# Kernel optimization log

Measured on AMD Instinct MI355X. Metric: run time of the kernel, lower is better.

The kernel has to match this reference:

```python
import jax, jax.numpy as jnp
import numpy as np

B, C, H, W = 32, 512, 64, 64
P = 8            # partition (window) size
HEAD_DIM = 32
N_HEADS = C // HEAD_DIM  # 16
MLP_RATIO = 4
LN_EPS = 1e-5


def _rel_pos_index(p):
    # Swin/MaxViT-style relative position index for a p x p window -> [p*p, p*p]
    coords = np.stack(np.meshgrid(np.arange(p), np.arange(p), indexing='ij'), 0).reshape(2, -1)
    rel = coords[:, :, None] - coords[:, None, :]          # [2, pp, pp]
    rel = rel.transpose(1, 2, 0) + (p - 1)                 # shift to >= 0
    idx = rel[..., 0] * (2 * p - 1) + rel[..., 1]          # [pp, pp]
    return jnp.asarray(idx, jnp.int32)


def setup_inputs() -> dict:
    key = jax.random.key(0)
    ks = jax.random.split(key, 10)
    s = 0.02
    d_ff = MLP_RATIO * C
    inp = {
        'x': jax.random.normal(ks[0], (B, C, H, W), jnp.float32),
        'gamma1': jnp.ones((C,), jnp.float32),
        'beta1': jnp.zeros((C,), jnp.float32),
        'gamma2': jnp.ones((C,), jnp.float32),
        'beta2': jnp.zeros((C,), jnp.float32),
        'qkv_w': jax.random.normal(ks[1], (C, 3 * C), jnp.float32) * s,
        'qkv_b': jnp.zeros((3 * C,), jnp.float32),
        'merge_w': jax.random.normal(ks[2], (C, C), jnp.float32) * s,
        'merge_b': jnp.zeros((C,), jnp.float32),
        'bias_table': jax.random.normal(ks[3], ((2 * P - 1) ** 2, N_HEADS), jnp.float32) * s,
        'w1': jax.random.normal(ks[4], (C, d_ff), jnp.float32) * s,
        'b1': jnp.zeros((d_ff,), jnp.float32),
        'w2': jax.random.normal(ks[5], (d_ff, C), jnp.float32) * s,
        'b2': jnp.zeros((C,), jnp.float32),
        'rel_idx': _rel_pos_index(P),
    }
    return inp


def _layernorm(t, g, b):
    mu = jnp.mean(t, axis=-1, keepdims=True)
    var = jnp.mean(jnp.square(t - mu), axis=-1, keepdims=True)
    return (t - mu) * jax.lax.rsqrt(var + LN_EPS) * g + b


def reference(x, gamma1, beta1, gamma2, beta2, qkv_w, qkv_b, merge_w, merge_b,
              bias_table, w1, b1, w2, b2, rel_idx):
    p, hd, nh = P, HEAD_DIM, N_HEADS
    Bx, Cx, Hx, Wx = x.shape
    hp, wp = Hx // p, Wx // p
    G, PP = hp * wp, p * p

    # --- window partition: [B,C,H,W] -> [B, G, p*p, C] (partition_type='window', no swap)
    xw = x.reshape(Bx, Cx, hp, p, wp, p).transpose(0, 2, 4, 3, 5, 1).reshape(Bx, G, PP, Cx)

    # --- relative-position multi-head attention on norm1(x)
    h = _layernorm(xw, gamma1, beta1)
    qkv = h @ qkv_w + qkv_b                                   # [B,G,PP,3C]
    q, k, v = jnp.split(qkv, 3, axis=-1)
    q = q.reshape(Bx, G, PP, nh, hd) * (hd ** -0.5)
    k = k.reshape(Bx, G, PP, nh, hd)
    v = v.reshape(Bx, G, PP, nh, hd)
    attn = jnp.einsum('bgqhd,bgkhd->bghqk', q, k)             # [B,G,nh,PP,PP]
    bias = bias_table[rel_idx]                                # [PP,PP,nh]
    attn = attn + bias.transpose(2, 0, 1)[None, None]
    attn = jax.nn.softmax(attn, axis=-1)
    o = jnp.einsum('bghqk,bgkhd->bgqhd', attn, v).reshape(Bx, G, PP, Cx)
    xw = xw + (o @ merge_w + merge_b)                          # residual (dropout/SD p=0)

    # --- MLP block on norm2(x)
    h2 = _layernorm(xw, gamma2, beta2)
    m = jax.nn.gelu(h2 @ w1 + b1) @ w2 + b2
    xw = xw + m

    # --- window departition: [B,G,p*p,C] -> [B,C,H,W]
    out = xw.reshape(Bx, hp, wp, p, p, Cx).transpose(0, 5, 1, 3, 2, 4).reshape(Bx, Cx, Hx, Wx)
    return out
```

## Files before the change

### kernel.cpp

```cpp
#include <hip/hip_runtime.h>
#include <stdint.h>

typedef __attribute__((ext_vector_type(8))) short short8;
typedef __attribute__((ext_vector_type(4))) float f32x4;
typedef __attribute__((address_space(3))) void lds_void;
typedef __attribute__((address_space(1))) void gv_void;

static __device__ __forceinline__ float bf2f(unsigned short u) {
    union { uint32_t i; float f; } v; v.i = ((uint32_t)u) << 16; return v.f;
}
static __device__ __forceinline__ unsigned short f2bf(float f) {
    union { float f; uint32_t i; } v; v.f = f;
    uint32_t i = v.i;
    uint32_t r = (i + 0x7fffu + ((i >> 16) & 1u)) >> 16;
    return (unsigned short)r;
}
static __device__ __forceinline__ float fexp(float x) {
    float r;
    asm("v_exp_f32 %0, %1" : "=v"(r) : "v"(x * 1.44269504088896f));
    return r;
}
static __device__ __forceinline__ float frcp(float x) {
    float r;
    asm("v_rcp_f32 %0, %1" : "=v"(r) : "v"(x));
    return r;
}
static __device__ __forceinline__ uint32_t cvtpk(float lo, float hi) {
    uint32_t r;
    asm("v_cvt_pk_bf16_f32 %0, %1, %2" : "=v"(r) : "v"(lo), "v"(hi));
    return r;
}

__global__ void k_detect(const void* __restrict__ g1, int* __restrict__ flag) {
    if (threadIdx.x == 0 && blockIdx.x == 0) {
        const unsigned short* u = (const unsigned short*)g1;
        flag[0] = (u[0] == 0x3F80u) ? 0 : 1;
    }
}

__global__ __launch_bounds__(256) void k_cvt(const void* __restrict__ src,
                                             unsigned short* __restrict__ dst,
                                             int n, const int* __restrict__ flag) {
    int i = blockIdx.x * 256 + threadIdx.x;
    if (i < n) {
        dst[i] = flag[0] ? f2bf(((const float*)src)[i])
                         : ((const unsigned short*)src)[i];
    }
}

__global__ __launch_bounds__(256) void k_transpose(const void* __restrict__ in,
                                                   unsigned short* __restrict__ out,
                                                   int R, int C, const int* __restrict__ flag) {
    __shared__ unsigned short tile[32][33];
    int isf = flag[0];
    int tx = threadIdx.x, ty = threadIdx.y;
    int x = blockIdx.x * 32 + tx;
    int y0 = blockIdx.y * 32;
    for (int j = ty; j < 32; j += 8) {
        size_t idx = (size_t)(y0 + j) * C + x;
        tile[j][tx] = isf ? f2bf(((const float*)in)[idx]) : ((const unsigned short*)in)[idx];
    }
    __syncthreads();
    int x2 = y0 + tx;
    int y20 = blockIdx.x * 32;
    for (int j = ty; j < 32; j += 8)
        out[(size_t)(y20 + j) * R + x2] = tile[tx][j];
}

__global__ __launch_bounds__(256) void k_prep_bias(const void* __restrict__ bias_table,
                                                   const int* __restrict__ rel_idx,
                                                   float* __restrict__ biasb,
                                                   const int* __restrict__ flag) {
    int i = blockIdx.x * 256 + threadIdx.x;
    int isf = flag[0];
    int r  = i & 3, rl = (i >> 2) & 15, qg = (i >> 6) & 3;
    int km = (i >> 8) & 3, qn = (i >> 10) & 3, h = (i >> 12) & 15;
    int q = 16 * qn + rl, k = 16 * km + 4 * qg + r;
    size_t idx = (size_t)rel_idx[q * 64 + k] * 16 + h;
    float v = isf ? ((const float*)bias_table)[idx] : bf2f(((const unsigned short*)bias_table)[idx]);
    biasb[i] = v;
}

__global__ __launch_bounds__(256) void k_partition_ln(const void* __restrict__ x,
                                                      const unsigned short* __restrict__ g1,
                                                      const unsigned short* __restrict__ b1,
                                                      unsigned short* __restrict__ xw,
                                                      unsigned short* __restrict__ h,
                                                      int b0, const int* __restrict__ flag) {
    __shared__ unsigned short tile[64][512];
    int isf = flag[0];
    int bh = blockIdx.x, bl = bh >> 6, hh = bh & 63;
    int b = b0 + bl;
    int tid = threadIdx.x;
    size_t xoff = (((size_t)b * 512) * 64 + hh) * 64;
    int c0 = tid >> 3, ch = tid & 7;
    if (isf) {
        const float* xb = (const float*)x + xoff;
        for (int k = 0; k < 16; ++k) {
            int c = c0 + k * 32;
            f32x4 v0 = *reinterpret_cast<const f32x4*>(xb + (size_t)c * 4096 + ch * 8);
            f32x4 v1 = *reinterpret_cast<const f32x4*>(xb + (size_t)c * 4096 + ch * 8 + 4);
#pragma unroll
            for (int j = 0; j < 4; ++j) tile[ch * 8 + j][c] = f2bf(v0[j]);
#pragma unroll
            for (int j = 0; j < 4; ++j) tile[ch * 8 + 4 + j][c] = f2bf(v1[j]);
        }
    } else {
        const unsigned short* xb = (const unsigned short*)x + xoff;
        for (int k = 0; k < 16; ++k) {
            int c = c0 + k * 32;
            short8 v = *reinterpret_cast<const short8*>(xb + (size_t)c * 4096 + ch * 8);
#pragma unroll
            for (int j = 0; j < 8; ++j) tile[ch * 8 + j][c] = (unsigned short)v[j];
        }
    }
    __syncthreads();
    int w = tid >> 2, q = tid & 3;
    float s = 0.f, s2 = 0.f;
#pragma unroll 4
    for (int j = 0; j < 128; ++j) {
        int c = q * 128 + ((j + 8 * w) & 127);
        float f = bf2f(tile[w][c]);
        s += f; s2 += f * f;
    }
    s += __shfl_xor(s, 1);  s += __shfl_xor(s, 2);
    s2 += __shfl_xor(s2, 1); s2 += __shfl_xor(s2, 2);
    float mu = s * (1.f / 512.f);
    float rstd = rsqrtf(s2 * (1.f / 512.f) - mu * mu + 1e-5f);
    int t = (bl * 64 + (hh >> 3) * 8 + (w >> 3)) * 64 + (hh & 7) * 8 + (w & 7);
    unsigned short* xr = xw + (size_t)t * 512;
    unsigned short* hr = h + (size_t)t * 512;
    for (int cc = q * 128; cc < q * 128 + 128; cc += 8) {
        short8 raw, hn;
#pragma unroll
        for (int j = 0; j < 8; ++j) {
            unsigned short u = tile[w][cc + j];
            raw[j] = (short)u;
            float f = (bf2f(u) - mu) * rstd * bf2f(g1[cc + j]) + bf2f(b1[cc + j]);
            hn[j] = (short)f2bf(f);
        }
        *reinterpret_cast<short8*>(xr + cc) = raw;
        *reinterpret_cast<short8*>(hr + cc) = hn;
    }
}

__global__ __launch_bounds__(256) void k_ln(const unsigned short* __restrict__ in,
                                            const unsigned short* __restrict__ g,
                                            const unsigned short* __restrict__ b,
                                            unsigned short* __restrict__ out) {
    int wid = threadIdx.x >> 6, lane = threadIdx.x & 63;
    size_t t = (size_t)blockIdx.x * 4 + wid;
    short8 v = *reinterpret_cast<const short8*>(in + t * 512 + lane * 8);
    float f[8], s = 0.f, s2 = 0.f;
#pragma unroll
    for (int j = 0; j < 8; ++j) { f[j] = bf2f((unsigned short)v[j]); s += f[j]; s2 += f[j] * f[j]; }
    for (int m = 1; m < 64; m <<= 1) { s += __shfl_xor(s, m); s2 += __shfl_xor(s2, m); }
    float mu = s * (1.f / 512.f);
    float rstd = rsqrtf(s2 * (1.f / 512.f) - mu * mu + 1e-5f);
    short8 ov;
#pragma unroll
    for (int j = 0; j < 8; ++j)
        ov[j] = (short)f2bf((f[j] - mu) * rstd * bf2f(g[lane * 8 + j]) + bf2f(b[lane * 8 + j]));
    *reinterpret_cast<short8*>(out + t * 512 + lane * 8) = ov;
}

template <int MODE>
__global__ __launch_bounds__(512, 1) void k_gemm7(const unsigned short* __restrict__ A,
                                                  const unsigned short* __restrict__ BT,
                                                  const unsigned short* __restrict__ bias,
                                                  const unsigned short* __restrict__ res,
                                                  unsigned short* __restrict__ out,
                                                  unsigned short* __restrict__ vt,
                                                  int M, int N, int K) {
    __shared__ unsigned short S[65536];
    const int tid = threadIdx.x, lane = tid & 63, wid = tid >> 6;

    int nwg = gridDim.x * gridDim.y;
    int lin = blockIdx.y * gridDim.x + blockIdx.x;
    int swz = (lin & 7) * (nwg >> 3) + (lin >> 3);
    int mt = swz % gridDim.x, nt = swz / gridDim.x;

    const int wr = wid >> 2, wc = wid & 3;
    const int rl = lane & 15, qg = lane >> 4;

    const int strow = tid >> 2;
    const int scb   = (tid & 3) ^ ((tid >> 3) & 3);
    const unsigned short* Agb = A  + ((size_t)mt * 256 + strow) * K + scb * 8;
    const unsigned short* Bgb = BT + ((size_t)nt * 256 + strow) * K + scb * 8;
    const int ldst = strow * 32 + (tid & 3) * 8;

    f32x4 acc[8][4];
#pragma unroll
    for (int mf = 0; mf < 8; ++mf)
#pragma unroll
        for (int nf = 0; nf < 4; ++nf) {
            acc[mf][nf][0] = 0.f; acc[mf][nf][1] = 0.f; acc[mf][nf][2] = 0.f; acc[mf][nf][3] = 0.f;
        }

    const int NH = K >> 5;

    auto stage = [&](int h) {
        int base = (h & 3) * 16384;
#pragma unroll
        for (int s = 0; s < 2; ++s) {
            __builtin_amdgcn_global_load_lds((const gv_void*)(Agb + (size_t)s * 128 * K + h * 32),
                                             (lds_void*)(&S[base + s * 4096 + ldst]), 16, 0, 0);
            __builtin_amdgcn_global_load_lds((const gv_void*)(Bgb + (size_t)s * 128 * K + h * 32),
                                             (lds_void*)(&S[base + 8192 + s * 4096 + ldst]), 16, 0, 0);
        }
    };

    const int arow0 = wr * 128 + rl;
    const int brow0 = wc * 64 + rl;
    const int kbr = (qg ^ ((rl >> 1) & 3)) * 8;

    auto readf = [&](int h, short8 (&af)[8], short8 (&bfr)[4]) {
        const unsigned short* sA = &S[(h & 3) * 16384];
        const unsigned short* sB = sA + 8192;
#pragma unroll
        for (int nf = 0; nf < 4; ++nf)
            bfr[nf] = *reinterpret_cast<const short8*>(&sB[(brow0 + nf * 16) * 32 + kbr]);
#pragma unroll
        for (int mf = 0; mf < 8; ++mf)
            af[mf] = *reinterpret_cast<const short8*>(&sA[(arow0 + mf * 16) * 32 + kbr]);
    };

    auto body = [&](int h, short8 (&uA)[8], short8 (&uB)[4],
                    short8 (&rA)[8], short8 (&rB)[4]) {
        if (h + 2 < NH)      { asm volatile("s_waitcnt vmcnt(4)" ::: "memory"); }
        else if (h + 1 < NH) { asm volatile("s_waitcnt vmcnt(0)" ::: "memory"); }
        __builtin_amdgcn_s_barrier();
        asm volatile("" ::: "memory");
        if (h + 3 < NH) stage(h + 3);
        if (h + 1 < NH) readf(h + 1, rA, rB);
        __builtin_amdgcn_s_setprio(1);
#pragma unroll
        for (int mf = 0; mf < 8; ++mf)
#pragma unroll
            for (int nf = 0; nf < 4; ++nf)
                acc[mf][nf] = __builtin_amdgcn_mfma_f32_16x16x32_bf16(uA[mf], uB[nf], acc[mf][nf], 0, 0, 0);
        __builtin_amdgcn_s_setprio(0);
    };

    stage(0); stage(1); stage(2);
    asm volatile("s_waitcnt vmcnt(8)" ::: "memory");
    __builtin_amdgcn_s_barrier();
    asm volatile("" ::: "memory");

    short8 afA[8], bfA[4], afB[8], bfB[4];
    readf(0, afA, bfA);

    for (int hh = 0; hh < NH; hh += 2) {
        body(hh,     afA, bfA, afB, bfB);
        body(hh + 1, afB, bfB, afA, bfA);
    }

    const int PST = 264;
    unsigned short* pb = (unsigned short*)S;
    float bz[4];
#pragma unroll
    for (int nf = 0; nf < 4; ++nf) bz[nf] = bf2f(bias[nt * 256 + wc * 64 + nf * 16 + rl]);
    int row_l = tid >> 4, cbl = (tid & 15) * 16;
    int growb = mt * 256 + (row_l >> 4) * 128 + (row_l & 15);
    size_t gcol = (size_t)nt * 256 + cbl;

#pragma unroll
    for (int mf = 0; mf < 8; ++mf) {
        __syncthreads();
#pragma unroll
        for (int nf = 0; nf < 4; ++nf)
#pragma unroll
            for (int r = 0; r < 4; ++r) {
                float v = acc[mf][nf][r] + bz[nf];
                if (MODE == 2) {
                    float z = 0.7978845608f * (v + 0.044715f * v * v * v);
                    float e = fexp(-2.0f * z);
                    v = v * frcp(1.f + e);
                }
                pb[(wr * 16 + qg * 4 + r) * PST + wc * 64 + nf * 16 + rl] = f2bf(v);
            }
        __syncthreads();

        size_t go = (size_t)(growb + mf * 16) * N + gcol;
        short8 o1 = *reinterpret_cast<const short8*>(&pb[row_l * PST + cbl]);
        short8 o2 = *reinterpret_cast<const short8*>(&pb[row_l * PST + cbl + 8]);
        if (MODE == 1) {
            short8 r1 = *reinterpret_cast<const short8*>(&res[go]);
            short8 r2 = *reinterpret_cast<const short8*>(&res[go + 8]);
#pragma unroll
            for (int j = 0; j < 8; ++j) {
                o1[j] = (short)f2bf(bf2f((unsigned short)o1[j]) + bf2f((unsigned short)r1[j]));
                o2[j] = (short)f2bf(bf2f((unsigned short)o2[j]) + bf2f((unsigned short)r2[j]));
            }
        }
        *reinterpret_cast<short8*>(&out[go]) = o1;
        *reinterpret_cast<short8*>(&out[go + 8]) = o2;

        if (MODE == 0 && nt >= 4) {
#pragma unroll
            for (int s = 0; s < 2; ++s) {
                int run = tid + 512 * s;
                int c = run & 255, hp = run >> 8, half = hp >> 1, ph = hp & 1;
                int prow = half * 16 + ph * 8;
                short8 v8;
#pragma unroll
                for (int i = 0; i < 8; ++i) v8[i] = (short)pb[(prow + i) * PST + c];
                int t0 = mt * 256 + half * 128 + mf * 16 + ph * 8;
                int cc = nt * 256 + c - 1024;
                int win = t0 >> 6, k0 = t0 & 63;
                *reinterpret_cast<short8*>(&vt[((size_t)(win * 16 + (cc >> 5)) * 32 + (cc & 31)) * 64 + k0]) = v8;
            }
        }
    }
}

__global__ __launch_bounds__(64) void k_attn2(const unsigned short* __restrict__ qkv,
                                              const unsigned short* __restrict__ vt,
                                              const float* __restrict__ biasb,
                                              unsigned short* __restrict__ o) {
    __shared__ unsigned short Pl[64 * 72];
    int blk = blockIdx.x;
    int head = blk & 15, win = blk >> 4;
    size_t T0 = (size_t)win * 64;
    int lane = threadIdx.x;
    int rl = lane & 15, qg = lane >> 4;
    const unsigned short* base = qkv + T0 * 1536;
    int qoff = head * 32, koff = 512 + head * 32;

    short8 kf[4], qf[4];
#pragma unroll
    for (int m = 0; m < 4; ++m) {
        kf[m] = *reinterpret_cast<const short8*>(base + (size_t)(16 * m + rl) * 1536 + koff + qg * 8);
        qf[m] = *reinterpret_cast<const short8*>(base + (size_t)(16 * m + rl) * 1536 + qoff + qg * 8);
    }
    f32x4 st[4][4];
#pragma unroll
    for (int km = 0; km < 4; ++km)
#pragma unroll
        for (int qn = 0; qn < 4; ++qn) { st[km][qn][0] = 0.f; st[km][qn][1] = 0.f; st[km][qn][2] = 0.f; st[km][qn][3] = 0.f; }
#pragma unroll
    for (int km = 0; km < 4; ++km)
#pragma unroll
        for (int qn = 0; qn < 4; ++qn)
            st[km][qn] = __builtin_amdgcn_mfma_f32_16x16x32_bf16(kf[km], qf[qn], st[km][qn], 0, 0, 0);

    const float scale = 0.17677669529663687f;
    const float* bh = biasb + head * 4096 + qg * 64 + rl * 4;
#pragma unroll
    for (int qn = 0; qn < 4; ++qn) {
        float vv[4][4];
        float mx = -3.0e38f;
#pragma unroll
        for (int km = 0; km < 4; ++km) {
            f32x4 b4 = *reinterpret_cast<const f32x4*>(bh + qn * 1024 + km * 256);
#pragma unroll
            for (int r = 0; r < 4; ++r) {
                vv[km][r] = st[km][qn][r] * scale + b4[r];
                mx = fmaxf(mx, vv[km][r]);
            }
        }
        mx = fmaxf(mx, __shfl_xor(mx, 16));
        mx = fmaxf(mx, __shfl_xor(mx, 32));
        float sm = 0.f;
#pragma unroll
        for (int km = 0; km < 4; ++km)
#pragma unroll
            for (int r = 0; r < 4; ++r) { vv[km][r] = fexp(vv[km][r] - mx); sm += vv[km][r]; }
        sm += __shfl_xor(sm, 16);
        sm += __shfl_xor(sm, 32);
        float inv = frcp(sm);
        int q = 16 * qn + rl;
#pragma unroll
        for (int km = 0; km < 4; ++km) {
            uint32_t w0 = cvtpk(vv[km][0] * inv, vv[km][1] * inv);
            uint32_t w1 = cvtpk(vv[km][2] * inv, vv[km][3] * inv);
            uint32_t* p = reinterpret_cast<uint32_t*>(&Pl[q * 72 + 16 * km + 4 * qg]);
            p[0] = w0; p[1] = w1;
        }
    }

    short8 vf[2][2];
    const unsigned short* vb = vt + (size_t)(win * 16 + head) * 2048;
#pragma unroll
    for (int kb = 0; kb < 2; ++kb)
#pragma unroll
        for (int dn = 0; dn < 2; ++dn)
            vf[kb][dn] = *reinterpret_cast<const short8*>(vb + (16 * dn + rl) * 64 + 32 * kb + 8 * qg);

    __syncthreads();

    f32x4 acc[4][2];
#pragma unroll
    for (int qm = 0; qm < 4; ++qm)
#pragma unroll
        for (int dn = 0; dn < 2; ++dn) { acc[qm][dn][0] = 0.f; acc[qm][dn][1] = 0.f; acc[qm][dn][2] = 0.f; acc[qm][dn][3] = 0.f; }

#pragma unroll
    for (int qm = 0; qm < 4; ++qm) {
        short8 a0 = *reinterpret_cast<const short8*>(&Pl[(16 * qm + rl) * 72 + 8 * qg]);
        short8 a1 = *reinterpret_cast<const short8*>(&Pl[(16 * qm + rl) * 72 + 32 + 8 * qg]);
#pragma unroll
        for (int dn = 0; dn < 2; ++dn) {
            acc[qm][dn] = __builtin_amdgcn_mfma_f32_16x16x32_bf16(a0, vf[0][dn], acc[qm][dn], 0, 0, 0);
            acc[qm][dn] = __builtin_amdgcn_mfma_f32_16x16x32_bf16(a1, vf[1][dn], acc[qm][dn], 0, 0, 0);
        }
    }
#pragma unroll
    for (int qm = 0; qm < 4; ++qm)
#pragma unroll
        for (int dn = 0; dn < 2; ++dn)
#pragma unroll
            for (int r = 0; r < 4; ++r)
                o[(T0 + 16 * qm + 4 * qg + r) * 512 + head * 32 + 16 * dn + rl] = f2bf(acc[qm][dn][r]);
}

__global__ __launch_bounds__(256) void k_departition(const unsigned short* __restrict__ tok,
                                                     void* __restrict__ xo,
                                                     int b0, const int* __restrict__ flag) {
    __shared__ unsigned short tile[64][512];
    int isf = flag[0];
    int bh = blockIdx.x, bl = bh >> 6, hh = bh & 63;
    int b = b0 + bl;
    int tid = threadIdx.x;
    int Tb = (bl * 64 + (hh >> 3) * 8) * 64 + (hh & 7) * 8;
    for (int k = 0; k < 16; ++k) {
        int flat = k * 256 + tid;
        int w = flat >> 6, ch = flat & 63;
        int t = Tb + (w >> 3) * 64 + (w & 7);
        short8 v = *reinterpret_cast<const short8*>(tok + (size_t)t * 512 + ch * 8);
        *reinterpret_cast<short8*>(&tile[w][ch * 8]) = v;
    }
    __syncthreads();
    size_t xoff = (((size_t)b * 512) * 64 + hh) * 64;
    if (isf) {
        float* xb = (float*)xo + xoff;
        for (int k = 0; k < 16; ++k) {
            int flat = k * 256 + tid;
            int c = flat >> 3, wc = flat & 7;
            f32x4 a, d;
#pragma unroll
            for (int j = 0; j < 4; ++j) a[j] = bf2f(tile[wc * 8 + j][c]);
#pragma unroll
            for (int j = 0; j < 4; ++j) d[j] = bf2f(tile[wc * 8 + 4 + j][c]);
            *reinterpret_cast<f32x4*>(xb + (size_t)c * 4096 + wc * 8) = a;
            *reinterpret_cast<f32x4*>(xb + (size_t)c * 4096 + wc * 8 + 4) = d;
        }
    } else {
        unsigned short* xb = (unsigned short*)xo + xoff;
        for (int k = 0; k < 16; ++k) {
            int flat = k * 256 + tid;
            int c = flat >> 3, wc = flat & 7;
            short8 v;
#pragma unroll
            for (int j = 0; j < 8; ++j) v[j] = (short)tile[wc * 8 + j][c];
            *reinterpret_cast<short8*>(xb + (size_t)c * 4096 + wc * 8) = v;
        }
    }
}

extern "C" void kernel_launch(void* const* d_in, const int* in_sizes, int n_in,
                              void* d_out, int out_size, void* d_ws, size_t ws_size,
                              hipStream_t stream) {
    const void* x          = d_in[0];
    const void* g1         = d_in[1];
    const void* be1        = d_in[2];
    const void* g2         = d_in[3];
    const void* be2        = d_in[4];
    const void* qkv_w      = d_in[5];
    const void* qkv_b      = d_in[6];
    const void* merge_w    = d_in[7];
    const void* merge_b    = d_in[8];
    const void* bias_table = d_in[9];
    const void* w1         = d_in[10];
    const void* b1         = d_in[11];
    const void* w2         = d_in[12];
    const void* b2         = d_in[13];
    const int*  rel_idx    = (const int*)d_in[14];

    const size_t extra = 8u << 20;
    int CB = 4;
    if (ws_size >= (size_t)32768 * 11264 + extra) CB = 8;
    int nch = 32 / CB;
    size_t tok = (size_t)CB * 4096;

    unsigned short* xw_c     = (unsigned short*)d_ws;
    unsigned short* h_c      = xw_c + tok * 512;
    unsigned short* o_c      = h_c + tok * 512;
    unsigned short* qkv_c    = o_c + tok * 512;
    unsigned short* mid_c    = qkv_c + tok * 1536;
    unsigned short* vt_c     = mid_c + tok * 2048;
    unsigned short* qkv_wT   = vt_c + tok * 512;
    unsigned short* merge_wT = qkv_wT + 1536 * 512;
    unsigned short* w1T      = merge_wT + 512 * 512;
    unsigned short* w2T      = w1T + 2048 * 512;
    unsigned short* vecs     = w2T + 512 * 2048;
    float*          biasb    = (float*)(vecs + 6656);
    int*            flag     = (int*)(biasb + 65536);

    unsigned short* ng1 = vecs + 0,    *nbe1 = vecs + 512;
    unsigned short* ng2 = vecs + 1024, *nbe2 = vecs + 1536;
    unsigned short* nqb = vecs + 2048, *nmb  = vecs + 3584;
    unsigned short* nb1 = vecs + 4096, *nb2  = vecs + 6144;

    k_detect<<<1, 64, 0, stream>>>(g1, flag);
    k_cvt<<<2, 256, 0, stream>>>(g1, ng1, 512, flag);
    k_cvt<<<2, 256, 0, stream>>>(be1, nbe1, 512, flag);
    k_cvt<<<2, 256, 0, stream>>>(g2, ng2, 512, flag);
    k_cvt<<<2, 256, 0, stream>>>(be2, nbe2, 512, flag);
    k_cvt<<<6, 256, 0, stream>>>(qkv_b, nqb, 1536, flag);
    k_cvt<<<2, 256, 0, stream>>>(merge_b, nmb, 512, flag);
    k_cvt<<<8, 256, 0, stream>>>(b1, nb1, 2048, flag);
    k_cvt<<<2, 256, 0, stream>>>(b2, nb2, 512, flag);
    k_transpose<<<dim3(48, 16), dim3(32, 8), 0, stream>>>(qkv_w, qkv_wT, 512, 1536, flag);
    k_transpose<<<dim3(16, 16), dim3(32, 8), 0, stream>>>(merge_w, merge_wT, 512, 512, flag);
    k_transpose<<<dim3(64, 16), dim3(32, 8), 0, stream>>>(w1, w1T, 512, 2048, flag);
    k_transpose<<<dim3(16, 64), dim3(32, 8), 0, stream>>>(w2, w2T, 2048, 512, flag);
    k_prep_bias<<<256, 256, 0, stream>>>(bias_table, rel_idx, biasb, flag);

    int mtiles = (int)(tok / 256);
    int M = (int)tok;
    for (int c = 0; c < nch; ++c) {
        int b0 = c * CB;
        k_partition_ln<<<CB * 64, 256, 0, stream>>>(x, ng1, nbe1, xw_c, h_c, b0, flag);
        k_gemm7<0><<<dim3(mtiles, 6), 512, 0, stream>>>(h_c, qkv_wT, nqb, nullptr, qkv_c, vt_c, M, 1536, 512);
        k_attn2<<<CB * 1024, 64, 0, stream>>>(qkv_c, vt_c, biasb, o_c);
        k_gemm7<1><<<dim3(mtiles, 2), 512, 0, stream>>>(o_c, merge_wT, nmb, xw_c, xw_c, nullptr, M, 512, 512);
        k_ln<<<(int)(tok / 4), 256, 0, stream>>>(xw_c, ng2, nbe2, h_c);
        k_gemm7<2><<<dim3(mtiles, 8), 512, 0, stream>>>(h_c, w1T, nb1, nullptr, mid_c, nullptr, M, 2048, 512);
        k_gemm7<1><<<dim3(mtiles, 2), 512, 0, stream>>>(mid_c, w2T, nb2, xw_c, qkv_c, nullptr, M, 512, 2048);
        k_departition<<<CB * 64, 256, 0, stream>>>(qkv_c, d_out, b0, flag);
    }
}
```

Baseline: 1.968 ms.

## Restructure GEMM main loop into two half-tile phases with split A/B staging

Replaces the register double-buffered GEMM loop, which prefetched all fragments of the next K-step, with a loop that splits each K-step into two halves of four M-fragments. Each half loads its own fragments from LDS and issues either the A or the B global->LDS stage, separated by barriers and sched_barriers. The aim is to cut register pressure and interleave LDS reads, global loads and MFMA more evenly. The trade-off is extra barriers per K-step and less overlap of LDS reads with MFMA, because fragments are no longer prefetched a whole step ahead.

```diff
diff --git a/kernel.cpp b/kernel.cpp
--- a/kernel.cpp
+++ b/kernel.cpp
@@ -165,7 +165,7 @@
 }
 
 template <int MODE>
-__global__ __launch_bounds__(512, 1) void k_gemm7(const unsigned short* __restrict__ A,
+__global__ __launch_bounds__(512, 1) void k_gemm8(const unsigned short* __restrict__ A,
                                                   const unsigned short* __restrict__ BT,
                                                   const unsigned short* __restrict__ bias,
                                                   const unsigned short* __restrict__ res,
@@ -199,60 +199,78 @@
 
     const int NH = K >> 5;
 
-    auto stage = [&](int h) {
+    auto stageA = [&](int h) {
         int base = (h & 3) * 16384;
 #pragma unroll
-        for (int s = 0; s < 2; ++s) {
+        for (int s = 0; s < 2; ++s)
             __builtin_amdgcn_global_load_lds((const gv_void*)(Agb + (size_t)s * 128 * K + h * 32),
                                              (lds_void*)(&S[base + s * 4096 + ldst]), 16, 0, 0);
+    };
+    auto stageB = [&](int h) {
+        int base = (h & 3) * 16384 + 8192;
+#pragma unroll
+        for (int s = 0; s < 2; ++s)
             __builtin_amdgcn_global_load_lds((const gv_void*)(Bgb + (size_t)s * 128 * K + h * 32),
-                                             (lds_void*)(&S[base + 8192 + s * 4096 + ldst]), 16, 0, 0);
-        }
+                                             (lds_void*)(&S[base + s * 4096 + ldst]), 16, 0, 0);
     };
+
+    stageA(0); stageB(0);
+    stageA(1); stageB(1);
+    stageA(2); stageB(2);
+    asm volatile("s_waitcnt vmcnt(8)" ::: "memory");
+    __builtin_amdgcn_s_barrier();
 
     const int arow0 = wr * 128 + rl;
     const int brow0 = wc * 64 + rl;
     const int kbr = (qg ^ ((rl >> 1) & 3)) * 8;
 
-    auto readf = [&](int h, short8 (&af)[8], short8 (&bfr)[4]) {
+    for (int h = 0; h < NH; ++h) {
         const unsigned short* sA = &S[(h & 3) * 16384];
         const unsigned short* sB = sA + 8192;
+
+        short8 af[4], bfr[4];
 #pragma unroll
         for (int nf = 0; nf < 4; ++nf)
             bfr[nf] = *reinterpret_cast<const short8*>(&sB[(brow0 + nf * 16) * 32 + kbr]);
 #pragma unroll
-        for (int mf = 0; mf < 8; ++mf)
-            af[mf] = *reinterpret_cast<const short8*>(&sA[(arow0 + mf * 16) * 32 + kbr]);
-    };
-
-    auto body = [&](int h, short8 (&uA)[8], short8 (&uB)[4],
-                    short8 (&rA)[8], short8 (&rB)[4]) {
-        if (h + 2 < NH)      { asm volatile("s_waitcnt vmcnt(4)" ::: "memory"); }
+        for (int i = 0; i < 4; ++i)
+            af[i] = *reinterpret_cast<const short8*>(&sA[(arow0 + i * 16) * 32 + kbr]);
+        __builtin_amdgcn_sched_barrier(0);
+        if (h + 3 < NH) stageA(h + 3);
+        __builtin_amdgcn_s_barrier();
+        asm volatile("s_waitcnt lgkmcnt(0)" ::: "memory");
+        __builtin_amdgcn_sched_barrier(0);
+        __builtin_amdgcn_s_setprio(1);
+#pragma unroll
+        for (int i = 0; i < 4; ++i)
+#pragma unroll
+            for (int nf = 0; nf < 4; ++nf)
+                acc[i][nf] = __builtin_amdgcn_mfma_f32_16x16x32_bf16(af[i], bfr[nf], acc[i][nf], 0, 0, 0);
+        __builtin_amdgcn_s_setprio(0);
+        __builtin_amdgcn_sched_barrier(0);
+        __builtin_amdgcn_s_barrier();
+
+        short8 ag[4];
+#pragma unroll
+        for (int i = 0; i < 4; ++i)
+            ag[i] = *reinterpret_cast<const short8*>(&sA[(arow0 + 64 + i * 16) * 32 + kbr]);
+        __builtin_amdgcn_sched_barrier(0);
+        if (h + 3 < NH) stageB(h + 3);
+        __builtin_amdgcn_s_barrier();
+        asm volatile("s_waitcnt lgkmcnt(0)" ::: "memory");
+        __builtin_amdgcn_sched_barrier(0);
+        __builtin_amdgcn_s_setprio(1);
+#pragma unroll
+        for (int i = 0; i < 4; ++i)
+#pragma unroll
+            for (int nf = 0; nf < 4; ++nf)
+                acc[4 + i][nf] = __builtin_amdgcn_mfma_f32_16x16x32_bf16(ag[i], bfr[nf], acc[4 + i][nf], 0, 0, 0);
+        __builtin_amdgcn_s_setprio(0);
+        __builtin_amdgcn_sched_barrier(0);
+        if (h + 3 < NH)      { asm volatile("s_waitcnt vmcnt(8)" ::: "memory"); }
+        else if (h + 2 < NH) { asm volatile("s_waitcnt vmcnt(4)" ::: "memory"); }
         else if (h + 1 < NH) { asm volatile("s_waitcnt vmcnt(0)" ::: "memory"); }
         __builtin_amdgcn_s_barrier();
-        asm volatile("" ::: "memory");
-        if (h + 3 < NH) stage(h + 3);
-        if (h + 1 < NH) readf(h + 1, rA, rB);
-        __builtin_amdgcn_s_setprio(1);
-#pragma unroll
-        for (int mf = 0; mf < 8; ++mf)
-#pragma unroll
-            for (int nf = 0; nf < 4; ++nf)
-                acc[mf][nf] = __builtin_amdgcn_mfma_f32_16x16x32_bf16(uA[mf], uB[nf], acc[mf][nf], 0, 0, 0);
-        __builtin_amdgcn_s_setprio(0);
-    };
-
-    stage(0); stage(1); stage(2);
-    asm volatile("s_waitcnt vmcnt(8)" ::: "memory");
-    __builtin_amdgcn_s_barrier();
-    asm volatile("" ::: "memory");
-
-    short8 afA[8], bfA[4], afB[8], bfB[4];
-    readf(0, afA, bfA);
-
-    for (int hh = 0; hh < NH; hh += 2) {
-        body(hh,     afA, bfA, afB, bfB);
-        body(hh + 1, afB, bfB, afA, bfA);
     }
 
     const int PST = 264;
@@ -522,12 +540,12 @@
     for (int c = 0; c < nch; ++c) {
         int b0 = c * CB;
         k_partition_ln<<<CB * 64, 256, 0, stream>>>(x, ng1, nbe1, xw_c, h_c, b0, flag);
-        k_gemm7<0><<<dim3(mtiles, 6), 512, 0, stream>>>(h_c, qkv_wT, nqb, nullptr, qkv_c, vt_c, M, 1536, 512);
+        k_gemm8<0><<<dim3(mtiles, 6), 512, 0, stream>>>(h_c, qkv_wT, nqb, nullptr, qkv_c, vt_c, M, 1536, 512);
         k_attn2<<<CB * 1024, 64, 0, stream>>>(qkv_c, vt_c, biasb, o_c);
-        k_gemm7<1><<<dim3(mtiles, 2), 512, 0, stream>>>(o_c, merge_wT, nmb, xw_c, xw_c, nullptr, M, 512, 512);
+        k_gemm8<1><<<dim3(mtiles, 2), 512, 0, stream>>>(o_c, merge_wT, nmb, xw_c, xw_c, nullptr, M, 512, 512);
         k_ln<<<(int)(tok / 4), 256, 0, stream>>>(xw_c, ng2, nbe2, h_c);
-        k_gemm7<2><<<dim3(mtiles, 8), 512, 0, stream>>>(h_c, w1T, nb1, nullptr, mid_c, nullptr, M, 2048, 512);
-        k_gemm7<1><<<dim3(mtiles, 2), 512, 0, stream>>>(mid_c, w2T, nb2, xw_c, qkv_c, nullptr, M, 512, 2048);
+        k_gemm8<2><<<dim3(mtiles, 8), 512, 0, stream>>>(h_c, w1T, nb1, nullptr, mid_c, nullptr, M, 2048, 512);
+        k_gemm8<1><<<dim3(mtiles, 2), 512, 0, stream>>>(mid_c, w2T, nb2, xw_c, qkv_c, nullptr, M, 512, 2048);
         k_departition<<<CB * 64, 256, 0, stream>>>(qkv_c, d_out, b0, flag);
     }
 }
```

Result: no change. 1.982 ms (+0.7%).
